# Performance work log

Hardware: AMD Instinct MI355X
Metric: run time of the kernel (lower is better)

The kernel has to match this reference:

```python
import jax, jax.numpy as jnp
import numpy as np

B, IN, OUT = 16384, 4096, 4096


def setup_inputs() -> dict:
    key = jax.random.key(0)
    k1, k2, k3 = jax.random.split(key, 3)
    x = jax.random.normal(k1, (B, IN), dtype=jnp.float32)
    full_precision = jax.random.normal(k2, (OUT, IN), dtype=jnp.float32) * 0.02
    bias = jax.random.normal(k3, (OUT,), dtype=jnp.float32) * 0.02
    return {"x": x, "full_precision": full_precision, "bias": bias}


def reference(x, full_precision, bias):
    # In-place param preprocessing from the torch module:
    # center each weight row, then clamp to [-1, 1].
    fp = full_precision - jnp.mean(full_precision, axis=1, keepdims=True)
    fp = jnp.clip(fp, -1.0, 1.0)
    # BinActive: sign of the activations (dropout_ratio == 0, so no dropout).
    xb = jnp.sign(x)
    # Binary weight: sign(fp) scaled by per-output-row mean absolute value.
    mean_val = jnp.mean(jnp.abs(fp), axis=1, keepdims=True)  # [OUT, 1]
    w = jnp.sign(fp) * mean_val                               # [OUT, IN]
    # Dense linear: [B, IN] @ [IN, OUT] + [OUT]
    return xb @ w.T + bias
```

## Files before the change

### kernel.cpp

```cpp
#include <hip/hip_runtime.h>
#include <cstdint>

#define B_SZ   16384
#define IN_SZ  4096
#define OUT_SZ 4096

typedef int   int4v   __attribute__((ext_vector_type(4)));

__device__ __forceinline__ int sgn8(float v) { return (v > 0.f) - (v < 0.f); }

__global__ __launch_bounds__(256) void wprep_kernel(const float* __restrict__ fp,
                                                    int8_t* __restrict__ wb,
                                                    float* __restrict__ alpha) {
    __shared__ float red[4];
    const int o = blockIdx.x;
    const int t = threadIdx.x;
    const float4* row = (const float4*)(fp + (size_t)o * IN_SZ);

    float4 v[4];
    float s = 0.f;
#pragma unroll
    for (int i = 0; i < 4; ++i) {
        v[i] = row[t + i * 256];
        s += (v[i].x + v[i].y) + (v[i].z + v[i].w);
    }
#pragma unroll
    for (int off = 32; off > 0; off >>= 1) s += __shfl_down(s, off, 64);
    if ((t & 63) == 0) red[t >> 6] = s;
    __syncthreads();
    const float mean = (red[0] + red[1] + red[2] + red[3]) * (1.f / IN_SZ);
    __syncthreads();

    int* wrow = (int*)(wb + (size_t)o * IN_SZ);
    float a = 0.f;
#pragma unroll
    for (int i = 0; i < 4; ++i) {
        const float dx = v[i].x - mean, dy = v[i].y - mean;
        const float dz = v[i].z - mean, dw = v[i].w - mean;
        a += fminf(fabsf(dx), 1.f) + fminf(fabsf(dy), 1.f)
           + fminf(fabsf(dz), 1.f) + fminf(fabsf(dw), 1.f);
        const int p = (sgn8(dx) & 0xff) | ((sgn8(dy) & 0xff) << 8)
                    | ((sgn8(dz) & 0xff) << 16) | (sgn8(dw) << 24);
        wrow[t + i * 256] = p;
    }
#pragma unroll
    for (int off = 32; off > 0; off >>= 1) a += __shfl_down(a, off, 64);
    if ((t & 63) == 0) red[t >> 6] = a;
    __syncthreads();
    if (t == 0) alpha[o] = (red[0] + red[1] + red[2] + red[3]) * (1.f / IN_SZ);
}

__global__ __launch_bounds__(256) void xprep_kernel(const float* __restrict__ x,
                                                    int8_t* __restrict__ xb) {
    const size_t i = (size_t)blockIdx.x * 256 + threadIdx.x;
    const float4 v = ((const float4*)x)[i];
    const int p = (sgn8(v.x) & 0xff) | ((sgn8(v.y) & 0xff) << 8)
                | ((sgn8(v.z) & 0xff) << 16) | (sgn8(v.w) << 24);
    ((int*)xb)[i] = p;
}

__global__ __launch_bounds__(256) void gemm_kernel(const int8_t* __restrict__ Xb,
                                                   const int8_t* __restrict__ Wb,
                                                   const float* __restrict__ alpha,
                                                   const float* __restrict__ bias,
                                                   float* __restrict__ out) {
    __shared__ __align__(16) int8_t As[128 * 64];
    __shared__ __align__(16) int8_t Bs[128 * 64];

    const int tid  = threadIdx.x;
    const int lane = tid & 63;
    const int wave = tid >> 6;
    const int tm = blockIdx.x;
    const int tn = blockIdx.y;
    const int wm = (wave >> 1) * 64;
    const int wn = (wave & 1) * 64;

    const int srow = lane >> 2;
    const int scol = (lane & 3) * 16;
    const int8_t* gA = Xb + (size_t)(tm * 128 + wave * 32 + srow) * IN_SZ + scol;
    const int8_t* gB = Wb + (size_t)(tn * 128 + wave * 32 + srow) * IN_SZ + scol;

    int4v acc[4][4] = {};

    const int lrow = lane & 15;
    const int lq16 = (lane >> 4) * 16;

    for (int k0 = 0; k0 < IN_SZ; k0 += 64) {
#pragma unroll
        for (int j = 0; j < 2; ++j) {
            __builtin_amdgcn_global_load_lds(
                (const __attribute__((address_space(1))) uint32_t*)(gA + k0 + (size_t)j * 16 * IN_SZ),
                (__attribute__((address_space(3))) uint32_t*)(As + (wave * 32 + j * 16) * 64),
                16, 0, 0);
            __builtin_amdgcn_global_load_lds(
                (const __attribute__((address_space(1))) uint32_t*)(gB + k0 + (size_t)j * 16 * IN_SZ),
                (__attribute__((address_space(3))) uint32_t*)(Bs + (wave * 32 + j * 16) * 64),
                16, 0, 0);
        }
        __syncthreads();

        int4v a[4], b[4];
#pragma unroll
        for (int i = 0; i < 4; ++i) {
            a[i] = *(const int4v*)(As + (wm + i * 16 + lrow) * 64 + lq16);
            b[i] = *(const int4v*)(Bs + (wn + i * 16 + lrow) * 64 + lq16);
        }
#pragma unroll
        for (int i = 0; i < 4; ++i)
#pragma unroll
            for (int j = 0; j < 4; ++j)
                acc[i][j] = __builtin_amdgcn_mfma_i32_16x16x64_i8(a[i], b[j], acc[i][j], 0, 0, 0);
        __syncthreads();
    }

    const int col  = lane & 15;
    const int rowq = (lane >> 4) * 4;
#pragma unroll
    for (int j = 0; j < 4; ++j) {
        const int o = tn * 128 + wn + j * 16 + col;
        const float al = alpha[o];
        const float bi = bias[o];
#pragma unroll
        for (int i = 0; i < 4; ++i) {
            const size_t m = (size_t)(tm * 128 + wm + i * 16 + rowq);
#pragma unroll
            for (int r = 0; r < 4; ++r)
                out[(m + r) * OUT_SZ + o] = al * (float)acc[i][j][r] + bi;
        }
    }
}

extern "C" void kernel_launch(void* const* d_in, const int* in_sizes, int n_in,
                              void* d_out, int out_size, void* d_ws, size_t ws_size,
                              hipStream_t stream) {
    const float* x    = (const float*)d_in[0];
    const float* fp   = (const float*)d_in[1];
    const float* bias = (const float*)d_in[2];
    float* out = (float*)d_out;

    int8_t* xb    = (int8_t*)d_ws;
    int8_t* wb    = xb + (size_t)B_SZ * IN_SZ;
    float*  alpha = (float*)(wb + (size_t)OUT_SZ * IN_SZ);

    hipLaunchKernelGGL(wprep_kernel, dim3(OUT_SZ), dim3(256), 0, stream, fp, wb, alpha);
    hipLaunchKernelGGL(xprep_kernel, dim3(B_SZ * IN_SZ / 1024), dim3(256), 0, stream, x, xb);
    hipLaunchKernelGGL(gemm_kernel, dim3(B_SZ / 128, OUT_SZ / 128), dim3(256), 0, stream,
                       xb, wb, alpha, bias, out);
}
```

Before: 942.3 us.

## Switch GEMM to 32x32x32 int8 MFMA tiles and widen xprep per thread

Replaces the 4x4 grid of 16x16x64 int8 MFMAs per wave with a 2x2 grid of 32x32x32 MFMAs over two k sub-steps. This reduces LDS fragment loads per k-step and uses the larger MFMA shape, which may issue more efficiently. The epilogue is remapped to the 32x32 accumulator layout. It also adds a 4-blocks-per-CU launch bound hint and has each xprep thread process two float4s.

```diff
diff --git a/kernel.cpp b/kernel.cpp
--- a/kernel.cpp
+++ b/kernel.cpp
@@ -5,7 +5,8 @@
 #define IN_SZ  4096
 #define OUT_SZ 4096
 
-typedef int   int4v   __attribute__((ext_vector_type(4)));
+typedef int int4v  __attribute__((ext_vector_type(4)));
+typedef int int16v __attribute__((ext_vector_type(16)));
 
 __device__ __forceinline__ int sgn8(float v) { return (v > 0.f) - (v < 0.f); }
 
@@ -52,18 +53,22 @@
 
 __global__ __launch_bounds__(256) void xprep_kernel(const float* __restrict__ x,
                                                     int8_t* __restrict__ xb) {
-    const size_t i = (size_t)blockIdx.x * 256 + threadIdx.x;
-    const float4 v = ((const float4*)x)[i];
-    const int p = (sgn8(v.x) & 0xff) | ((sgn8(v.y) & 0xff) << 8)
-                | ((sgn8(v.z) & 0xff) << 16) | (sgn8(v.w) << 24);
-    ((int*)xb)[i] = p;
+    const size_t i = ((size_t)blockIdx.x * 256 + threadIdx.x) * 2;
+    const float4 v0 = ((const float4*)x)[i];
+    const float4 v1 = ((const float4*)x)[i + 1];
+    int2 p;
+    p.x = (sgn8(v0.x) & 0xff) | ((sgn8(v0.y) & 0xff) << 8)
+        | ((sgn8(v0.z) & 0xff) << 16) | (sgn8(v0.w) << 24);
+    p.y = (sgn8(v1.x) & 0xff) | ((sgn8(v1.y) & 0xff) << 8)
+        | ((sgn8(v1.z) & 0xff) << 16) | (sgn8(v1.w) << 24);
+    ((int2*)xb)[i / 2] = p;
 }
 
-__global__ __launch_bounds__(256) void gemm_kernel(const int8_t* __restrict__ Xb,
-                                                   const int8_t* __restrict__ Wb,
-                                                   const float* __restrict__ alpha,
-                                                   const float* __restrict__ bias,
-                                                   float* __restrict__ out) {
+__global__ __launch_bounds__(256, 4) void gemm_kernel(const int8_t* __restrict__ Xb,
+                                                      const int8_t* __restrict__ Wb,
+                                                      const float* __restrict__ alpha,
+                                                      const float* __restrict__ bias,
+                                                      float* __restrict__ out) {
     __shared__ __align__(16) int8_t As[128 * 64];
     __shared__ __align__(16) int8_t Bs[128 * 64];
 
@@ -80,10 +85,10 @@
     const int8_t* gA = Xb + (size_t)(tm * 128 + wave * 32 + srow) * IN_SZ + scol;
     const int8_t* gB = Wb + (size_t)(tn * 128 + wave * 32 + srow) * IN_SZ + scol;
 
-    int4v acc[4][4] = {};
+    int16v acc[2][2] = {};
 
-    const int lrow = lane & 15;
-    const int lq16 = (lane >> 4) * 16;
+    const int frow = lane & 31;
+    const int fk   = (lane >> 5) * 16;
 
     for (int k0 = 0; k0 < IN_SZ; k0 += 64) {
 #pragma unroll
@@ -99,33 +104,38 @@
         }
         __syncthreads();
 
-        int4v a[4], b[4];
 #pragma unroll
-        for (int i = 0; i < 4; ++i) {
-            a[i] = *(const int4v*)(As + (wm + i * 16 + lrow) * 64 + lq16);
-            b[i] = *(const int4v*)(Bs + (wn + i * 16 + lrow) * 64 + lq16);
+        for (int s = 0; s < 2; ++s) {
+            int4v a[2], b[2];
+#pragma unroll
+            for (int i = 0; i < 2; ++i) {
+                a[i] = *(const int4v*)(As + (wm + i * 32 + frow) * 64 + s * 32 + fk);
+                b[i] = *(const int4v*)(Bs + (wn + i * 32 + frow) * 64 + s * 32 + fk);
+            }
+#pragma unroll
+            for (int i = 0; i < 2; ++i)
+#pragma unroll
+                for (int j = 0; j < 2; ++j)
+                    acc[i][j] = __builtin_amdgcn_mfma_i32_32x32x32_i8(a[i], b[j], acc[i][j], 0, 0, 0);
         }
-#pragma unroll
-        for (int i = 0; i < 4; ++i)
-#pragma unroll
-            for (int j = 0; j < 4; ++j)
-                acc[i][j] = __builtin_amdgcn_mfma_i32_16x16x64_i8(a[i], b[j], acc[i][j], 0, 0, 0);
         __syncthreads();
     }
 
-    const int col  = lane & 15;
-    const int rowq = (lane >> 4) * 4;
+    const int col = lane & 31;
+    const int rbase = 4 * (lane >> 5);
 #pragma unroll
-    for (int j = 0; j < 4; ++j) {
-        const int o = tn * 128 + wn + j * 16 + col;
+    for (int j = 0; j < 2; ++j) {
+        const int o = tn * 128 + wn + j * 32 + col;
         const float al = alpha[o];
         const float bi = bias[o];
 #pragma unroll
-        for (int i = 0; i < 4; ++i) {
-            const size_t m = (size_t)(tm * 128 + wm + i * 16 + rowq);
+        for (int i = 0; i < 2; ++i) {
+            const size_t mbase = (size_t)(tm * 128 + wm + i * 32);
 #pragma unroll
-            for (int r = 0; r < 4; ++r)
-                out[(m + r) * OUT_SZ + o] = al * (float)acc[i][j][r] + bi;
+            for (int r = 0; r < 16; ++r) {
+                const int row = (r & 3) + 8 * (r >> 2) + rbase;
+                out[(mbase + row) * OUT_SZ + o] = al * (float)acc[i][j][r] + bi;
+            }
         }
     }
 }
@@ -143,7 +153,7 @@
     float*  alpha = (float*)(wb + (size_t)OUT_SZ * IN_SZ);
 
     hipLaunchKernelGGL(wprep_kernel, dim3(OUT_SZ), dim3(256), 0, stream, fp, wb, alpha);
-    hipLaunchKernelGGL(xprep_kernel, dim3(B_SZ * IN_SZ / 1024), dim3(256), 0, stream, x, xb);
+    hipLaunchKernelGGL(xprep_kernel, dim3(B_SZ * IN_SZ / 2048), dim3(256), 0, stream, x, xb);
     hipLaunchKernelGGL(gemm_kernel, dim3(B_SZ / 128, OUT_SZ / 128), dim3(256), 0, stream,
                        xb, wb, alpha, bias, out);
 }
```

Result: faster. 814.0 us (-13.6%).
